# Optimization experiments

Measured on AMD Instinct MI355X. Metric: run time of the kernel, lower is better.

Reference implementation:

```python
import jax, jax.numpy as jnp
import numpy as np

H = 1024   # hidden_size
V = 32000  # output_size (vocab)
L = 3      # num_decoder_layers
B = 64     # batch
T = 32     # max_length


def setup_inputs() -> dict:
    key = jax.random.key(0)
    ks = jax.random.split(key, 10)
    s = 1.0 / np.sqrt(H)
    u = lambda k, shape: jax.random.uniform(k, shape, jnp.float32, -s, s)
    return {
        "encoder_outputs": jax.random.normal(ks[0], (B, T, H), jnp.float32),
        "encoder_hidden": jax.random.normal(ks[1], (L, B, H), jnp.float32),
        "target_tensor": jax.random.randint(ks[2], (B, T), 0, V),
        "emb": u(ks[3], (V, H)),
        "W_ih": u(ks[4], (L, 3 * H, H)),
        "W_hh": u(ks[5], (L, 3 * H, H)),
        "b_ih": u(ks[6], (L, 3 * H)),
        "b_hh": u(ks[7], (L, 3 * H)),
        "W_out": u(ks[8], (V, H)),
        "b_out": u(ks[9], (V,)),
    }


def _gru_layer(x, h0, Wih, Whh, bih, bhh):
    # x: [B,T,H], h0: [B,H]; PyTorch GRU gate order: r, z, n
    xp = jnp.einsum('bth,gh->btg', x, Wih) + bih  # [B,T,3H], input projections hoisted out of scan

    def step(h, xpt):
        hp = h @ Whh.T + bhh  # [B,3H]
        r = jax.nn.sigmoid(xpt[:, :H] + hp[:, :H])
        z = jax.nn.sigmoid(xpt[:, H:2 * H] + hp[:, H:2 * H])
        n = jnp.tanh(xpt[:, 2 * H:] + r * hp[:, 2 * H:])
        hn = (1.0 - z) * n + z * h
        return hn, hn

    hT, ys = jax.lax.scan(step, h0, jnp.swapaxes(xp, 0, 1))  # time-major scan
    return jnp.swapaxes(ys, 0, 1), hT  # [B,T,H], [B,H]


def reference(encoder_outputs, encoder_hidden, target_tensor, emb, W_ih, W_hh, b_ih, b_hh, W_out, b_out):
    # Teacher forcing: step 0 consumes SOS token 0, step i consumes target[:, i-1]
    ids = jnp.concatenate([jnp.zeros((B, 1), target_tensor.dtype), target_tensor[:, :-1]], axis=1)  # [B,T]
    x = jax.nn.relu(emb[ids])  # [B,T,H]
    finals = []
    for l in range(L):  # small fixed layer loop
        x, hT = _gru_layer(x, encoder_hidden[l], W_ih[l], W_hh[l], b_ih[l], b_hh[l])
        finals.append(hT)
    logits = jnp.einsum('bth,vh->btv', x, W_out) + b_out  # [B,T,V]
    log_probs = jax.nn.log_softmax(logits, axis=-1)
    return log_probs, jnp.stack(finals, axis=0)
```

## Files before the change

kernel.cpp:

```cpp
#include <hip/hip_runtime.h>
#include <hip/hip_bf16.h>
#include <cstdint>
#include <cstddef>

#define Hdim 1024
#define Vdim 32000
#define LAYERS 3
#define Bdim 64
#define Tdim 32
#define BT 2048
#define G3H 3072

using bf16 = __bf16;
using bf16x8 = __attribute__((ext_vector_type(8))) __bf16;
using bf16x4 = __attribute__((ext_vector_type(4))) __bf16;
using f32x4  = __attribute__((ext_vector_type(4))) float;
using u32x4  = __attribute__((ext_vector_type(4))) unsigned int;

typedef const __attribute__((address_space(1))) void* gas1_t;
typedef __attribute__((address_space(3))) void* las3_t;
__device__ __forceinline__ void g2lds16(const void* g, void* l) {
  __builtin_amdgcn_global_load_lds((gas1_t)g, (las3_t)l, 16, 0, 0);
}

__global__ __launch_bounds__(256) void cvt_f32_bf16(const float* __restrict__ src,
                                                    bf16* __restrict__ dst, int n4) {
  int i = blockIdx.x * 256 + threadIdx.x;
  if (i < n4) {
    f32x4 v = ((const f32x4*)src)[i];
    bf16x4 o;
    o[0] = (bf16)v[0]; o[1] = (bf16)v[1]; o[2] = (bf16)v[2]; o[3] = (bf16)v[3];
    ((bf16x4*)dst)[i] = o;
  }
}

__global__ __launch_bounds__(256) void embed_relu(const int* __restrict__ tgt,
                                                  const float* __restrict__ emb,
                                                  bf16* __restrict__ x) {
  int row = blockIdx.x;
  int b = row >> 5, t = row & 31;
  int id = (t == 0) ? 0 : tgt[b * Tdim + t - 1];
  const f32x4* src = (const f32x4*)(emb + (size_t)id * Hdim);
  bf16x4* dst = (bf16x4*)(x + (size_t)row * Hdim);
  f32x4 v = src[threadIdx.x];
  bf16x4 o;
  o[0] = (bf16)fmaxf(v[0], 0.f); o[1] = (bf16)fmaxf(v[1], 0.f);
  o[2] = (bf16)fmaxf(v[2], 0.f); o[3] = (bf16)fmaxf(v[3], 0.f);
  dst[threadIdx.x] = o;
}

__global__ __launch_bounds__(256) void hinit(const float* __restrict__ eh,
                                             bf16* __restrict__ hbf,
                                             unsigned int* __restrict__ ctr) {
  if (blockIdx.x == 0 && threadIdx.x == 0) *ctr = 0u;
  int i = blockIdx.x * 256 + threadIdx.x;
  f32x4 v = ((const f32x4*)eh)[i];
  bf16x4 o;
  o[0] = (bf16)v[0]; o[1] = (bf16)v[1]; o[2] = (bf16)v[2]; o[3] = (bf16)v[3];
  ((bf16x4*)hbf)[i] = o;
}

template <bool BIAS>
__global__ __launch_bounds__(256) void gemm_lds(const bf16* __restrict__ A,
                                                const bf16* __restrict__ Bm,
                                                const float* __restrict__ bias,
                                                float* __restrict__ C,
                                                int M, int N, int K) {
  __shared__ bf16 As[128 * 32];
  __shared__ bf16 Bs[128 * 32];

  int wave = threadIdx.x >> 6, lane = threadIdx.x & 63;
  int lane15 = lane & 15, quad = lane >> 4;
  int wr = wave >> 1, wc = wave & 1;

  int flat = blockIdx.y * gridDim.x + blockIdx.x;
  int per = (gridDim.x * gridDim.y) >> 3;
  int nid = (flat & 7) * per + (flat >> 3);
  int mt = nid % gridDim.x;
  int nt = nid / gridDim.x;
  int m0 = mt * 128;
  int n0 = nt * 128;

  int srow = wave * 16 + (lane >> 2);
  int scol = (lane & 3) * 8;
  const bf16* Asrc = A + (size_t)(m0 + srow) * K + scol;
  const bf16* Bsrc = Bm + (size_t)(n0 + srow) * K + scol;
  bf16* AdstW = As + (size_t)wave * 512;
  bf16* BdstW = Bs + (size_t)wave * 512;

  f32x4 acc[4][4] = {};
  for (int k0 = 0; k0 < K; k0 += 32) {
#pragma unroll
    for (int r = 0; r < 2; r++) {
      g2lds16(Asrc + (size_t)(r * 64) * K + k0, AdstW + r * 2048);
      g2lds16(Bsrc + (size_t)(r * 64) * K + k0, BdstW + r * 2048);
    }
    __syncthreads();

    bf16x8 a[4], b[4];
#pragma unroll
    for (int mi = 0; mi < 4; mi++)
      a[mi] = *(const bf16x8*)&As[(wr * 64 + mi * 16 + lane15) * 32 + quad * 8];
#pragma unroll
    for (int ni = 0; ni < 4; ni++)
      b[ni] = *(const bf16x8*)&Bs[(wc * 64 + ni * 16 + lane15) * 32 + quad * 8];
#pragma unroll
    for (int mi = 0; mi < 4; mi++)
#pragma unroll
      for (int ni = 0; ni < 4; ni++)
        acc[mi][ni] = __builtin_amdgcn_mfma_f32_16x16x32_bf16(a[mi], b[ni], acc[mi][ni], 0, 0, 0);
    __syncthreads();
  }

#pragma unroll
  for (int mi = 0; mi < 4; mi++)
#pragma unroll
    for (int ni = 0; ni < 4; ni++) {
      int col = n0 + wc * 64 + ni * 16 + lane15;
      float bv = BIAS ? bias[col] : 0.f;
#pragma unroll
      for (int r = 0; r < 4; r++) {
        int row = m0 + wr * 64 + mi * 16 + quad * 4 + r;
        C[(size_t)row * N + col] = acc[mi][ni][r] + bv;
      }
    }
}

__global__ __launch_bounds__(256, 1) void gru_layer(
    const float* __restrict__ eh,
    const bf16* __restrict__ Whh,
    const float* __restrict__ bhh,
    const float* __restrict__ xp,
    bf16* hbfa,
    bf16* hbfb,
    bf16* __restrict__ y,
    float* __restrict__ finals,
    unsigned int* ctr) {
  extern __shared__ uint8_t smem_raw[];
  bf16* Wl = (bf16*)smem_raw;
  float* part = (float*)(smem_raw + 98304);

  int tid = threadIdx.x;
  int wave = tid >> 6, lane = tid & 63;
  int lane15 = lane & 15, quad = lane >> 4;
  int bid = blockIdx.x;
  int i0 = (bid & 63) * 16;
  int b0 = (bid >> 6) * 16;
  int kbase = wave * 256;

  {
    const bf16* Wb = Whh + (size_t)(i0 + lane15) * Hdim + kbase + quad * 8;
#pragma unroll
    for (int g = 0; g < 3; g++)
#pragma unroll
      for (int j = 0; j < 8; j++) {
        bf16x8 w = *(const bf16x8*)(Wb + (size_t)g * Hdim * Hdim + j * 32);
        *(bf16x8*)(Wl + ((((size_t)wave * 3 + g) * 8 + j) * 64 + lane) * 8) = w;
      }
  }

  int b_local = tid >> 4, i_local = tid & 15;
  int i_out = i0 + i_local;
  int b_out = b0 + b_local;
  float bhr = bhh[i_out], bhz = bhh[Hdim + i_out], bhn = bhh[2 * Hdim + i_out];
  size_t hi = (size_t)b_out * Hdim + i_out;
  float hold = eh[hi];
  const float* xpr = xp + ((size_t)b_out * Tdim) * G3H;

  __syncthreads();

  unsigned int target = 0;
  for (int t = 0; t < Tdim; t++) {
    const bf16* hp = (t & 1) ? hbfb : hbfa;
    bf16*       hn_ = (t & 1) ? hbfa : hbfb;

    float xr = xpr[(size_t)t * G3H + i_out];
    float xz = xpr[(size_t)t * G3H + Hdim + i_out];
    float xn = xpr[(size_t)t * G3H + 2 * Hdim + i_out];

    const bf16* Ap = hp + (size_t)(b0 + lane15) * Hdim + kbase + quad * 8;
    bf16x8 a[8];
#pragma unroll
    for (int j = 0; j < 8; j++) {
      u32x4 raw = *(volatile const u32x4*)(Ap + j * 32);
      a[j] = __builtin_bit_cast(bf16x8, raw);
    }

    f32x4 ar = {}, az = {}, an = {};
#pragma unroll
    for (int j = 0; j < 8; j++) {
      const bf16* wbase = Wl + (((size_t)wave * 3) * 8 + j) * 64 * 8 + lane * 8;
      bf16x8 wr8 = *(const bf16x8*)(wbase);
      bf16x8 wz8 = *(const bf16x8*)(wbase + 8 * 64 * 8);
      bf16x8 wn8 = *(const bf16x8*)(wbase + 16 * 64 * 8);
      ar = __builtin_amdgcn_mfma_f32_16x16x32_bf16(a[j], wr8, ar, 0, 0, 0);
      az = __builtin_amdgcn_mfma_f32_16x16x32_bf16(a[j], wz8, az, 0, 0, 0);
      an = __builtin_amdgcn_mfma_f32_16x16x32_bf16(a[j], wn8, an, 0, 0, 0);
    }
#pragma unroll
    for (int r = 0; r < 4; r++) {
      int idx = (quad * 4 + r) * 16 + lane15;
      part[(0 * 4 + wave) * 256 + idx] = ar[r];
      part[(1 * 4 + wave) * 256 + idx] = az[r];
      part[(2 * 4 + wave) * 256 + idx] = an[r];
    }
    __syncthreads();

    float hr = part[0 * 1024 + 0 * 256 + tid] + part[0 * 1024 + 1 * 256 + tid]
             + part[0 * 1024 + 2 * 256 + tid] + part[0 * 1024 + 3 * 256 + tid] + bhr;
    float hz = part[1 * 1024 + 0 * 256 + tid] + part[1 * 1024 + 1 * 256 + tid]
             + part[1 * 1024 + 2 * 256 + tid] + part[1 * 1024 + 3 * 256 + tid] + bhz;
    float hnp = part[2 * 1024 + 0 * 256 + tid] + part[2 * 1024 + 1 * 256 + tid]
              + part[2 * 1024 + 2 * 256 + tid] + part[2 * 1024 + 3 * 256 + tid] + bhn;
    float rg = 1.f / (1.f + __expf(-(xr + hr)));
    float zg = 1.f / (1.f + __expf(-(xz + hz)));
    float ng = tanhf(xn + rg * hnp);
    float hnew = (1.f - zg) * ng + zg * hold;
    hold = hnew;
    unsigned short us = __builtin_bit_cast(unsigned short, (bf16)hnew);
    ((volatile unsigned short*)hn_)[hi] = us;
    y[((size_t)b_out * Tdim + t) * Hdim + i_out] = (bf16)hnew;

    __syncthreads();
    target += 256;
    if (tid == 0) {
      __hip_atomic_fetch_add(ctr, 1u, __ATOMIC_RELAXED, __HIP_MEMORY_SCOPE_AGENT);
      while (__hip_atomic_load(ctr, __ATOMIC_RELAXED, __HIP_MEMORY_SCOPE_AGENT) < target)
        __builtin_amdgcn_s_sleep(1);
    }
    __syncthreads();
  }
  finals[hi] = hold;
}

__global__ __launch_bounds__(256) void logsoftmax(float* __restrict__ out) {
  __shared__ float sm[256], ss[256];
  int row = blockIdx.x;
  f32x4* x = (f32x4*)(out + (size_t)row * Vdim);
  const int n4 = Vdim / 4;
  float m = -1e30f, s = 0.f;
  for (int j = threadIdx.x; j < n4; j += 256) {
    f32x4 v = x[j];
    float vm = fmaxf(fmaxf(v[0], v[1]), fmaxf(v[2], v[3]));
    float nm = fmaxf(m, vm);
    s = s * __expf(m - nm) + __expf(v[0] - nm) + __expf(v[1] - nm)
                           + __expf(v[2] - nm) + __expf(v[3] - nm);
    m = nm;
  }
  sm[threadIdx.x] = m; ss[threadIdx.x] = s;
  __syncthreads();
  for (int off = 128; off; off >>= 1) {
    if (threadIdx.x < off) {
      float m1 = sm[threadIdx.x], s1 = ss[threadIdx.x];
      float m2 = sm[threadIdx.x + off], s2 = ss[threadIdx.x + off];
      float mm = fmaxf(m1, m2);
      sm[threadIdx.x] = mm;
      ss[threadIdx.x] = s1 * __expf(m1 - mm) + s2 * __expf(m2 - mm);
    }
    __syncthreads();
  }
  float lse = sm[0] + logf(ss[0]);
  for (int j = threadIdx.x; j < n4; j += 256) {
    f32x4 v = x[j];
    v[0] -= lse; v[1] -= lse; v[2] -= lse; v[3] -= lse;
    x[j] = v;
  }
}

extern "C" void kernel_launch(void* const* d_in, const int* in_sizes, int n_in,
                              void* d_out, int out_size, void* d_ws, size_t ws_size,
                              hipStream_t stream) {
  const float* enc_hidden = (const float*)d_in[1];
  const int*   target     = (const int*)d_in[2];
  const float* emb        = (const float*)d_in[3];
  const float* W_ih       = (const float*)d_in[4];
  const float* W_hh       = (const float*)d_in[5];
  const float* b_ih       = (const float*)d_in[6];
  const float* b_hh       = (const float*)d_in[7];
  const float* W_out      = (const float*)d_in[8];
  const float* b_out      = (const float*)d_in[9];

  float* out = (float*)d_out;
  float* finals = out + (size_t)BT * Vdim;

  uint8_t* wsp = (uint8_t*)d_ws;
  auto alloc = [&](size_t bytes) {
    uint8_t* p = wsp;
    wsp += (bytes + 255) & ~(size_t)255;
    return p;
  };
  bf16* wih_bf  = (bf16*)alloc((size_t)LAYERS * G3H * Hdim * 2);
  bf16* whh_bf  = (bf16*)alloc((size_t)LAYERS * G3H * Hdim * 2);
  bf16* wout_bf = (bf16*)alloc((size_t)Vdim * Hdim * 2);
  bf16* xA      = (bf16*)alloc((size_t)BT * Hdim * 2);
  bf16* xB      = (bf16*)alloc((size_t)BT * Hdim * 2);
  float* xp     = (float*)alloc((size_t)BT * G3H * 4);
  bf16* hbfa    = (bf16*)alloc((size_t)Bdim * Hdim * 2);
  bf16* hbfb    = (bf16*)alloc((size_t)Bdim * Hdim * 2);
  unsigned int* ctr = (unsigned int*)alloc(256);

  {
    int n4 = LAYERS * G3H * Hdim / 4;
    cvt_f32_bf16<<<(n4 + 255) / 256, 256, 0, stream>>>(W_ih, wih_bf, n4);
    cvt_f32_bf16<<<(n4 + 255) / 256, 256, 0, stream>>>(W_hh, whh_bf, n4);
    int m4 = Vdim * Hdim / 4;
    cvt_f32_bf16<<<(m4 + 255) / 256, 256, 0, stream>>>(W_out, wout_bf, m4);
  }

  embed_relu<<<BT, 256, 0, stream>>>(target, emb, xA);

  bf16* xin = xA;
  bf16* xout_ = xB;
  for (int l = 0; l < LAYERS; l++) {
    const float* eh_l = enc_hidden + (size_t)l * Bdim * Hdim;
    hinit<<<64, 256, 0, stream>>>(eh_l, hbfa, ctr);
    dim3 g1(BT / 128, G3H / 128);
    gemm_lds<true><<<g1, 256, 0, stream>>>(xin, wih_bf + (size_t)l * G3H * Hdim,
                                           b_ih + (size_t)l * G3H, xp, BT, G3H, Hdim);
    gru_layer<<<256, 256, 110592, stream>>>(eh_l,
                                            whh_bf + (size_t)l * G3H * Hdim,
                                            b_hh + (size_t)l * G3H, xp,
                                            hbfa, hbfb, xout_,
                                            finals + (size_t)l * Bdim * Hdim, ctr);
    bf16* tmp = xin; xin = xout_; xout_ = tmp;
  }

  dim3 g2(BT / 128, Vdim / 128);
  gemm_lds<true><<<g2, 256, 0, stream>>>(xin, wout_bf, b_out, out, BT, Vdim, Hdim);

  logsoftmax<<<BT, 256, 0, stream>>>(out);
}
```

Baseline: 1.581 ms.

## Use hierarchical per-batch-group barriers, prefetch gate inputs, swizzle GEMM LDS tiles

The grid-wide atomic barrier in the recurrent GRU kernel is replaced by a two-level barrier per batch group of 64 blocks. Each block only needs the hidden-state rows written by blocks in its own group, so the groups no longer wait on each other, and contention on a single counter is split across sub-counters. The next step's input-projection values are loaded before the reduction so their latency overlaps the barrier. Separately, the bf16 GEMM now uses an XOR-swizzled LDS column layout to cut bank conflicts; this needs a larger counter buffer and more careful counter initialisation.

Measured after the change: 1.407 ms. -11.0%, faster.

```diff
diff --git a/kernel.cpp b/kernel.cpp
--- a/kernel.cpp
+++ b/kernel.cpp
@@ -52,8 +52,8 @@
 __global__ __launch_bounds__(256) void hinit(const float* __restrict__ eh,
                                              bf16* __restrict__ hbf,
                                              unsigned int* __restrict__ ctr) {
-  if (blockIdx.x == 0 && threadIdx.x == 0) *ctr = 0u;
   int i = blockIdx.x * 256 + threadIdx.x;
+  if (i < 4096) ctr[i] = 0u;
   f32x4 v = ((const f32x4*)eh)[i];
   bf16x4 o;
   o[0] = (bf16)v[0]; o[1] = (bf16)v[1]; o[2] = (bf16)v[2]; o[3] = (bf16)v[3];
@@ -82,12 +82,14 @@
   int n0 = nt * 128;
 
   int srow = wave * 16 + (lane >> 2);
-  int scol = (lane & 3) * 8;
+  int scol = (((lane & 3) ^ ((srow >> 1) & 3)) * 8);
   const bf16* Asrc = A + (size_t)(m0 + srow) * K + scol;
   const bf16* Bsrc = Bm + (size_t)(n0 + srow) * K + scol;
   bf16* AdstW = As + (size_t)wave * 512;
   bf16* BdstW = Bs + (size_t)wave * 512;
 
+  int rslot = (quad ^ ((lane15 >> 1) & 3)) * 8;
+
   f32x4 acc[4][4] = {};
   for (int k0 = 0; k0 < K; k0 += 32) {
 #pragma unroll
@@ -100,10 +102,10 @@
     bf16x8 a[4], b[4];
 #pragma unroll
     for (int mi = 0; mi < 4; mi++)
-      a[mi] = *(const bf16x8*)&As[(wr * 64 + mi * 16 + lane15) * 32 + quad * 8];
+      a[mi] = *(const bf16x8*)&As[(wr * 64 + mi * 16 + lane15) * 32 + rslot];
 #pragma unroll
     for (int ni = 0; ni < 4; ni++)
-      b[ni] = *(const bf16x8*)&Bs[(wc * 64 + ni * 16 + lane15) * 32 + quad * 8];
+      b[ni] = *(const bf16x8*)&Bs[(wc * 64 + ni * 16 + lane15) * 32 + rslot];
 #pragma unroll
     for (int mi = 0; mi < 4; mi++)
 #pragma unroll
@@ -148,6 +150,10 @@
   int b0 = (bid >> 6) * 16;
   int kbase = wave * 256;
 
+  int group = bid >> 6;
+  unsigned int* subc  = ctr + (size_t)(group * 16 + (bid & 7)) * 64;
+  unsigned int* rootc = ctr + (size_t)(group * 16 + 8) * 64;
+
   {
     const bf16* Wb = Whh + (size_t)(i0 + lane15) * Hdim + kbase + quad * 8;
 #pragma unroll
@@ -167,16 +173,16 @@
   float hold = eh[hi];
   const float* xpr = xp + ((size_t)b_out * Tdim) * G3H;
 
+  float xr = xpr[i_out];
+  float xz = xpr[Hdim + i_out];
+  float xn = xpr[2 * Hdim + i_out];
+
   __syncthreads();
 
-  unsigned int target = 0;
+  unsigned int roottarget = 0;
   for (int t = 0; t < Tdim; t++) {
     const bf16* hp = (t & 1) ? hbfb : hbfa;
     bf16*       hn_ = (t & 1) ? hbfa : hbfb;
-
-    float xr = xpr[(size_t)t * G3H + i_out];
-    float xz = xpr[(size_t)t * G3H + Hdim + i_out];
-    float xn = xpr[(size_t)t * G3H + 2 * Hdim + i_out];
 
     const bf16* Ap = hp + (size_t)(b0 + lane15) * Hdim + kbase + quad * 8;
     bf16x8 a[8];
@@ -203,6 +209,13 @@
       part[(0 * 4 + wave) * 256 + idx] = ar[r];
       part[(1 * 4 + wave) * 256 + idx] = az[r];
       part[(2 * 4 + wave) * 256 + idx] = an[r];
+    }
+
+    float xr2 = 0.f, xz2 = 0.f, xn2 = 0.f;
+    if (t + 1 < Tdim) {
+      xr2 = xpr[(size_t)(t + 1) * G3H + i_out];
+      xz2 = xpr[(size_t)(t + 1) * G3H + Hdim + i_out];
+      xn2 = xpr[(size_t)(t + 1) * G3H + 2 * Hdim + i_out];
     }
     __syncthreads();
 
@@ -221,11 +234,16 @@
     ((volatile unsigned short*)hn_)[hi] = us;
     y[((size_t)b_out * Tdim + t) * Hdim + i_out] = (bf16)hnew;
 
-    __syncthreads();
-    target += 256;
+    xr = xr2; xz = xz2; xn = xn2;
+
+    __syncthreads();
+    roottarget += 8;
     if (tid == 0) {
-      __hip_atomic_fetch_add(ctr, 1u, __ATOMIC_RELAXED, __HIP_MEMORY_SCOPE_AGENT);
-      while (__hip_atomic_load(ctr, __ATOMIC_RELAXED, __HIP_MEMORY_SCOPE_AGENT) < target)
+      unsigned int old = __hip_atomic_fetch_add(subc, 1u, __ATOMIC_RELAXED,
+                                                __HIP_MEMORY_SCOPE_AGENT);
+      if ((old & 7) == 7)
+        __hip_atomic_fetch_add(rootc, 1u, __ATOMIC_RELAXED, __HIP_MEMORY_SCOPE_AGENT);
+      while (__hip_atomic_load(rootc, __ATOMIC_RELAXED, __HIP_MEMORY_SCOPE_AGENT) < roottarget)
         __builtin_amdgcn_s_sleep(1);
     }
     __syncthreads();
@@ -297,7 +315,7 @@
   float* xp     = (float*)alloc((size_t)BT * G3H * 4);
   bf16* hbfa    = (bf16*)alloc((size_t)Bdim * Hdim * 2);
   bf16* hbfb    = (bf16*)alloc((size_t)Bdim * Hdim * 2);
-  unsigned int* ctr = (unsigned int*)alloc(256);
+  unsigned int* ctr = (unsigned int*)alloc(16384);
 
   {
     int n4 = LAYERS * G3H * Hdim / 4;
```
